# Kernel optimization log

Hardware: AMD Instinct MI355X
Metric: run time of the kernel (lower is better)

## Reference

```python
import jax, jax.numpy as jnp
import numpy as np

EMBED_DIM = 1024
NUM_HEADS = 16
HEAD_DIM = EMBED_DIM // NUM_HEADS
MLP_HIDDEN = 4096


def layer_norm(x, gamma, beta, eps=1e-5):
    mu = jnp.mean(x, axis=-1, keepdims=True)
    var = jnp.var(x, axis=-1, keepdims=True)
    return (x - mu) / jnp.sqrt(var + eps) * gamma + beta


def setup_inputs() -> dict:
    key = jax.random.key(0)
    ks = jax.random.split(key, 16)
    d, h = EMBED_DIM, MLP_HIDDEN
    s = 0.02
    inp = {
        "x": jax.random.normal(ks[0], (2, 2048, d), dtype=jnp.float32),
        "ln1_g": jnp.ones((d,), jnp.float32),
        "ln1_b": jnp.zeros((d,), jnp.float32),
        "ln2_g": jnp.ones((d,), jnp.float32),
        "ln2_b": jnp.zeros((d,), jnp.float32),
        "Wq": jax.random.normal(ks[1], (d, d), jnp.float32) * s,
        "bq": jnp.zeros((d,), jnp.float32),
        "Wk": jax.random.normal(ks[2], (d, d), jnp.float32) * s,
        "bk": jnp.zeros((d,), jnp.float32),
        "Wv": jax.random.normal(ks[3], (d, d), jnp.float32) * s,
        "bv": jnp.zeros((d,), jnp.float32),
        "Wo": jax.random.normal(ks[4], (d, d), jnp.float32) * s,
        "bo": jnp.zeros((d,), jnp.float32),
        "W1": jax.random.normal(ks[5], (d, h), jnp.float32) * s,
        "b1": jnp.zeros((h,), jnp.float32),
        "W2": jax.random.normal(ks[6], (h, d), jnp.float32) * s,
        "b2": jnp.zeros((d,), jnp.float32),
    }
    return inp


def reference(x, ln1_g, ln1_b, ln2_g, ln2_b, Wq, bq, Wk, bk, Wv, bv, Wo, bo, W1, b1, W2, b2):
    B, T, C = x.shape
    H, Dh = NUM_HEADS, HEAD_DIM
    # attention branch
    xn = layer_norm(x, ln1_g, ln1_b)
    q = (xn @ Wq + bq).reshape(B, T, H, Dh).transpose(0, 2, 1, 3)  # [B,H,T,Dh]
    k = (xn @ Wk + bk).reshape(B, T, H, Dh).transpose(0, 2, 1, 3)
    v = (xn @ Wv + bv).reshape(B, T, H, Dh).transpose(0, 2, 1, 3)
    scores = jnp.einsum('bhtd,bhsd->bhts', q, k) / jnp.sqrt(jnp.float32(Dh))
    attn = jax.nn.softmax(scores, axis=-1)
    out = jnp.einsum('bhts,bhsd->bhtd', attn, v)
    out = out.transpose(0, 2, 1, 3).reshape(B, T, C)
    x = x + out @ Wo + bo
    # MLP branch
    xn2 = layer_norm(x, ln2_g, ln2_b)
    x = x + jax.nn.relu(xn2 @ W1 + b1) @ W2 + b2
    return x
```

## Files before the change

kernel.cpp:

```cpp
#include <hip/hip_runtime.h>

typedef float f32x4 __attribute__((ext_vector_type(4)));
typedef __bf16 bf16x8 __attribute__((ext_vector_type(8)));

constexpr int TT   = 2048;
constexpr int CC   = 1024;
constexpr int HIDN = 4096;
constexpr int MM   = 4096;
constexpr int NQKV = 3072;

union U84 { uint32_t u[4]; bf16x8 v; };

__device__ inline uint32_t cvt_pk_bf16(float lo, float hi) {
  uint32_t r;
  asm("v_cvt_pk_bf16_f32 %0, %1, %2" : "=v"(r) : "v"(lo), "v"(hi));
  return r;
}
__device__ inline ushort f2bf(float f) { return (ushort)(cvt_pk_bf16(f, 0.f) & 0xffffu); }
__device__ inline float bfbits2f(uint32_t bits) {
  union { uint32_t u; float f; } c; c.u = bits; return c.f;
}
__device__ inline float exp2_fast(float x) {
  float r;
  asm("v_exp_f32 %0, %1" : "=v"(r) : "v"(x));
  return r;
}

#define AS1C(p) ((__attribute__((address_space(1))) void*)(p))
#define AS3(p)  ((__attribute__((address_space(3))) void*)(p))

__global__ __launch_bounds__(256) void prep_weights(const float* __restrict__ Wq,
                                                    const float* __restrict__ Wk,
                                                    const float* __restrict__ Wv,
                                                    const float* __restrict__ Wo,
                                                    const float* __restrict__ W1,
                                                    const float* __restrict__ W2,
                                                    const float* __restrict__ bq,
                                                    const float* __restrict__ bk,
                                                    const float* __restrict__ bv,
                                                    const float* __restrict__ x,
                                                    const float* __restrict__ g1,
                                                    const float* __restrict__ b1v,
                                                    ushort* __restrict__ WqkvT,
                                                    ushort* __restrict__ WoT,
                                                    ushort* __restrict__ W1T,
                                                    ushort* __restrict__ W2T,
                                                    float* __restrict__ Bqkv,
                                                    ushort* __restrict__ Xn) {
  const int id = blockIdx.x;
  const int t = threadIdx.x;
  if (id >= 12300) {
    const int row = id - 12300;
    float4 v = reinterpret_cast<const float4*>(x + (size_t)row * CC)[t];
    float s  = v.x + v.y + v.z + v.w;
    float ss = v.x * v.x + v.y * v.y + v.z * v.z + v.w * v.w;
#pragma unroll
    for (int off = 32; off; off >>= 1) {
      s  += __shfl_down(s, off);
      ss += __shfl_down(ss, off);
    }
    __shared__ float red[16];
    const int wid = t >> 6, lane = t & 63;
    if (lane == 0) { red[wid] = s; red[8 + wid] = ss; }
    __syncthreads();
    if (t == 0) {
      red[0] = red[0] + red[1] + red[2] + red[3];
      red[8] = red[8] + red[9] + red[10] + red[11];
    }
    __syncthreads();
    const float mu   = red[0] * (1.0f / CC);
    const float var  = red[8] * (1.0f / CC) - mu * mu;
    const float rstd = rsqrtf(var + 1e-5f);
    float4 gg = reinterpret_cast<const float4*>(g1)[t];
    float4 bb = reinterpret_cast<const float4*>(b1v)[t];
    uint2 st;
    st.x = cvt_pk_bf16((v.x - mu) * rstd * gg.x + bb.x, (v.y - mu) * rstd * gg.y + bb.y);
    st.y = cvt_pk_bf16((v.z - mu) * rstd * gg.z + bb.z, (v.w - mu) * rstd * gg.w + bb.w);
    *reinterpret_cast<uint2*>(Xn + (size_t)row * CC + t * 4) = st;
    return;
  }
  if (id >= 12288) {
    const int i = (id - 12288) * 256 + t;
    Bqkv[i] = (i < 1024) ? bq[i] : ((i < 2048) ? bk[i - 1024] : bv[i - 2048]);
    return;
  }
  const float* W; ushort* out; int Kd, Nd, bx, by, rowOff = 0;
  if (id < 4096) {
    const int which = id >> 10, sub = id & 1023;
    bx = sub & 31; by = sub >> 5; Kd = 1024; Nd = 1024;
    if (which == 0)      { W = Wq; out = WqkvT; rowOff = 0; }
    else if (which == 1) { W = Wk; out = WqkvT; rowOff = 1024; }
    else if (which == 2) { W = Wv; out = WqkvT; rowOff = 2048; }
    else                 { W = Wo; out = WoT; }
  } else if (id < 8192) {
    const int sub = id - 4096; bx = sub & 127; by = sub >> 7;
    W = W1; out = W1T; Kd = 1024; Nd = 4096;
  } else {
    const int sub = id - 8192; bx = sub & 31; by = sub >> 5;
    W = W2; out = W2T; Kd = 4096; Nd = 1024;
  }
  const int n0 = bx * 32, k0 = by * 32;
  __shared__ float Ts[32][33];
  {
    const int r = t >> 3, cb = (t & 7) * 4;
    float4 v = *reinterpret_cast<const float4*>(W + (size_t)(k0 + r) * Nd + n0 + cb);
    Ts[r][cb + 0] = v.x; Ts[r][cb + 1] = v.y; Ts[r][cb + 2] = v.z; Ts[r][cb + 3] = v.w;
  }
  __syncthreads();
  {
    const int nl = t >> 3, kb = (t & 7) * 4;
    uint2 st;
    st.x = cvt_pk_bf16(Ts[kb + 0][nl], Ts[kb + 1][nl]);
    st.y = cvt_pk_bf16(Ts[kb + 2][nl], Ts[kb + 3][nl]);
    *reinterpret_cast<uint2*>(out + (size_t)(rowOff + n0 + nl) * Kd + k0 + kb) = st;
  }
}

template <bool RELU, bool VOUT, bool PARTIAL>
__global__ __launch_bounds__(512, 2) void gemm_8w(const ushort* __restrict__ A,
                                                  const ushort* __restrict__ Bt,
                                                  const float* __restrict__ bias,
                                                  ushort* __restrict__ outp,
                                                  ushort* __restrict__ Vt,
                                                  ushort* __restrict__ P1,
                                                  ushort* __restrict__ P2,
                                                  ushort* __restrict__ P3,
                                                  int N, int K, int Kchunk) {
  __shared__ ushort lds[49152];
  const int t = threadIdx.x, lane = t & 63, w = t >> 6;
  const int g = lane >> 4, i16 = lane & 15;
  const int wr = w >> 2, wc = w & 3;
  const int nwg  = gridDim.x * gridDim.y;
  const int orig = blockIdx.y * gridDim.x + blockIdx.x;
  const int sw   = (orig & 7) * (nwg >> 3) + (orig >> 3);
  const int row0 = (sw / gridDim.x) * 256, col0 = (sw % gridDim.x) * 256;
  const int kstart = PARTIAL ? blockIdx.z * Kchunk : 0;
  const int NT = (PARTIAL ? Kchunk : K) >> 5;
  ushort* __restrict__ Out = outp;
  if (PARTIAL) Out = (blockIdx.z == 0) ? outp : (blockIdx.z == 1) ? P1
              : (blockIdx.z == 2) ? P2 : P3;

  const int c1 = t, c2 = t + 512;
  const int r1 = c1 >> 2, s1 = (c1 & 3) ^ ((r1 >> 1) & 3);
  const int r2 = c2 >> 2, s2 = (c2 & 3) ^ ((r2 >> 1) & 3);
  const ushort* aG1 = A + (size_t)(row0 + r1) * K + kstart + s1 * 8;
  const ushort* aG2 = A + (size_t)(row0 + r2) * K + kstart + s2 * 8;
  const ushort* bG1 = Bt + (size_t)(col0 + r1) * K + kstart + s1 * 8;
  const ushort* bG2 = Bt + (size_t)(col0 + r2) * K + kstart + s2 * 8;

  int aoff[8], boff[4];
#pragma unroll
  for (int mf = 0; mf < 8; ++mf) {
    const int R = wr * 128 + mf * 16 + i16;
    aoff[mf] = R * 64 + ((g ^ ((R >> 1) & 3)) << 4);
  }
#pragma unroll
  for (int nf = 0; nf < 4; ++nf) {
    const int Cn = wc * 64 + nf * 16 + i16;
    boff[nf] = Cn * 64 + ((g ^ ((Cn >> 1) & 3)) << 4);
  }

  f32x4 acc[8][4] = {};

  auto STAGE = [&](int bi, int kt) {
    char* aB = (char*)lds + bi * 32768;
    char* bB = aB + 16384;
    const int ko = kt * 32;
    __builtin_amdgcn_global_load_lds(AS1C(aG1 + ko), AS3(aB + w * 1024), 16, 0, 0);
    __builtin_amdgcn_global_load_lds(AS1C(aG2 + ko), AS3(aB + 8192 + w * 1024), 16, 0, 0);
    __builtin_amdgcn_global_load_lds(AS1C(bG1 + ko), AS3(bB + w * 1024), 16, 0, 0);
    __builtin_amdgcn_global_load_lds(AS1C(bG2 + ko), AS3(bB + 8192 + w * 1024), 16, 0, 0);
  };

  STAGE(0, 0);
  if (NT > 1) STAGE(1, 1);

  for (int kt = 0; kt < NT; ++kt) {
    const int cur = kt % 3;
    if (kt + 2 < NT) STAGE((kt + 2) % 3, kt + 2);
    if (kt + 2 < NT)      asm volatile("s_waitcnt vmcnt(8)" ::: "memory");
    else if (kt + 1 < NT) asm volatile("s_waitcnt vmcnt(4)" ::: "memory");
    else                  asm volatile("s_waitcnt vmcnt(0)" ::: "memory");
    asm volatile("s_barrier" ::: "memory");
    __builtin_amdgcn_sched_barrier(0);

    const char* aB = (const char*)lds + cur * 32768;
    const char* bB = aB + 16384;
    bf16x8 b4[4], a4[4];
#pragma unroll
    for (int nf = 0; nf < 4; ++nf) b4[nf] = *reinterpret_cast<const bf16x8*>(bB + boff[nf]);
#pragma unroll
    for (int mf = 0; mf < 4; ++mf) a4[mf] = *reinterpret_cast<const bf16x8*>(aB + aoff[mf]);
    __builtin_amdgcn_s_setprio(1);
#pragma unroll
    for (int mf = 0; mf < 4; ++mf)
#pragma unroll
      for (int nf = 0; nf < 4; ++nf)
        acc[mf][nf] = __builtin_amdgcn_mfma_f32_16x16x32_bf16(a4[mf], b4[nf], acc[mf][nf], 0, 0, 0);
    __builtin_amdgcn_s_setprio(0);
    asm volatile("s_barrier" ::: "memory");
    __builtin_amdgcn_sched_barrier(0);
#pragma unroll
    for (int mf = 0; mf < 4; ++mf) a4[mf] = *reinterpret_cast<const bf16x8*>(aB + aoff[mf + 4]);
    __builtin_amdgcn_s_setprio(1);
#pragma unroll
    for (int mf = 0; mf < 4; ++mf)
#pragma unroll
      for (int nf = 0; nf < 4; ++nf)
        acc[mf + 4][nf] = __builtin_amdgcn_mfma_f32_16x16x32_bf16(a4[mf], b4[nf], acc[mf + 4][nf], 0, 0, 0);
    __builtin_amdgcn_s_setprio(0);
    asm volatile("s_barrier" ::: "memory");
    __builtin_amdgcn_sched_barrier(0);
  }

  const int qcol0 = col0 + wc * 64;

  if (VOUT && qcol0 >= 2048) {
#pragma unroll
    for (int nf = 0; nf < 4; ++nf) {
      const int ncol = qcol0 + nf * 16 + i16;
      const float bb = bias[ncol];
      const int d = ncol - 2048;
      const int hh = d >> 6, dd = d & 63;
#pragma unroll
      for (int mf = 0; mf < 8; ++mf) {
        const int mrow = row0 + wr * 128 + mf * 16 + 4 * g;
        const int bb_ = mrow >> 11, tok = mrow & 2047;
        uint2 st;
        st.x = cvt_pk_bf16(acc[mf][nf][0] + bb, acc[mf][nf][1] + bb);
        st.y = cvt_pk_bf16(acc[mf][nf][2] + bb, acc[mf][nf][3] + bb);
        *reinterpret_cast<uint2*>(Vt + (size_t)((bb_ * 16 + hh) * 64 + dd) * TT + tok) = st;
      }
    }
    return;
  }

  float* Lf = (float*)((char*)lds + w * 4096);
  const int rr2 = lane >> 2, q = lane & 3;
#pragma unroll
  for (int mf = 0; mf < 8; ++mf) {
#pragma unroll
    for (int nf = 0; nf < 4; ++nf)
#pragma unroll
      for (int r = 0; r < 4; ++r) {
        const int row = 4 * g + r;
        Lf[row * 64 + ((16 * nf + i16) ^ ((row & 7) << 2))] = acc[mf][nf][r];
      }
    asm volatile("s_waitcnt lgkmcnt(0)" ::: "memory");
    uint32_t u[8];
#pragma unroll
    for (int j = 0; j < 4; ++j) {
      f32x4 v = *reinterpret_cast<const f32x4*>(Lf + rr2 * 64 + ((q * 16 + 4 * j) ^ ((rr2 & 7) << 2)));
      float e0 = v[0], e1 = v[1], e2 = v[2], e3 = v[3];
      if (!PARTIAL) {
        const float4 b4 = *reinterpret_cast<const float4*>(bias + qcol0 + q * 16 + 4 * j);
        e0 += b4.x; e1 += b4.y; e2 += b4.z; e3 += b4.w;
        if (RELU) {
          e0 = fmaxf(e0, 0.f); e1 = fmaxf(e1, 0.f);
          e2 = fmaxf(e2, 0.f); e3 = fmaxf(e3, 0.f);
        }
      }
      u[2 * j + 0] = cvt_pk_bf16(e0, e1);
      u[2 * j + 1] = cvt_pk_bf16(e2, e3);
    }
    const int mrow = row0 + wr * 128 + mf * 16 + rr2;
    ushort* orow = Out + (size_t)mrow * N + qcol0 + q * 16;
    uint4 s0; s0.x = u[0]; s0.y = u[1]; s0.z = u[2]; s0.w = u[3];
    uint4 s1; s1.x = u[4]; s1.y = u[5]; s1.z = u[6]; s1.w = u[7];
    *reinterpret_cast<uint4*>(orow) = s0;
    *reinterpret_cast<uint4*>(orow + 8) = s1;
    asm volatile("s_waitcnt lgkmcnt(0)" ::: "memory");
  }
}

__global__ __launch_bounds__(256) void gemm_splitk(const ushort* __restrict__ A,
                                                   const ushort* __restrict__ Bt,
                                                   ushort* __restrict__ P0,
                                                   ushort* __restrict__ P1,
                                                   ushort* __restrict__ P2,
                                                   ushort* __restrict__ P3,
                                                   int N, int K, int Kchunk) {
  __shared__ ushort Smem[8192];
  ushort* Asm = Smem;
  ushort* Bsm = Smem + 4096;
  const int t = threadIdx.x;
  const int lane = t & 63, w = t >> 6;
  const int g = lane >> 4, i16 = lane & 15;
  const int wrow = w >> 1, wcol = w & 1;
  const int nwg  = gridDim.x * gridDim.y;
  const int orig = blockIdx.y * gridDim.x + blockIdx.x;
  const int sw   = (orig & 7) * (nwg >> 3) + (orig >> 3);
  const int row0 = (sw / gridDim.x) * 128, col0 = (sw % gridDim.x) * 128;
  const int kstart = blockIdx.z * Kchunk;
  ushort* __restrict__ P = (blockIdx.z == 0) ? P0 : (blockIdx.z == 1) ? P1
                          : (blockIdx.z == 2) ? P2 : P3;

  f32x4 acc[4][4] = {};

  const int srow = t >> 2, sc = (t & 3) * 8;
  const ushort* aS1 = A + (size_t)(row0 + srow) * K + sc;
  const ushort* aS2 = A + (size_t)(row0 + 64 + srow) * K + sc;
  const ushort* bS1 = Bt + (size_t)(col0 + srow) * K + sc;
  const ushort* bS2 = Bt + (size_t)(col0 + 64 + srow) * K + sc;
  char* aL1 = (char*)Asm + w * 1024;
  char* aL2 = (char*)Asm + 4096 + w * 1024;
  char* bL1 = (char*)Bsm + w * 1024;
  char* bL2 = (char*)Bsm + 4096 + w * 1024;

  for (int k0 = kstart; k0 < kstart + Kchunk; k0 += 32) {
    __syncthreads();
    __builtin_amdgcn_global_load_lds(AS1C(aS1 + k0), AS3(aL1), 16, 0, 0);
    __builtin_amdgcn_global_load_lds(AS1C(aS2 + k0), AS3(aL2), 16, 0, 0);
    __builtin_amdgcn_global_load_lds(AS1C(bS1 + k0), AS3(bL1), 16, 0, 0);
    __builtin_amdgcn_global_load_lds(AS1C(bS2 + k0), AS3(bL2), 16, 0, 0);
    __syncthreads();

    bf16x8 a4[4], b4[4];
#pragma unroll
    for (int mf = 0; mf < 4; ++mf) {
      const int r = wrow * 64 + mf * 16 + i16;
      a4[mf] = *reinterpret_cast<const bf16x8*>((const char*)Asm + r * 64 + g * 16);
    }
#pragma unroll
    for (int nf = 0; nf < 4; ++nf) {
      const int c = wcol * 64 + nf * 16 + i16;
      b4[nf] = *reinterpret_cast<const bf16x8*>((const char*)Bsm + c * 64 + g * 16);
    }
#pragma unroll
    for (int mf = 0; mf < 4; ++mf)
#pragma unroll
      for (int nf = 0; nf < 4; ++nf)
        acc[mf][nf] = __builtin_amdgcn_mfma_f32_16x16x32_bf16(a4[mf], b4[nf], acc[mf][nf], 0, 0, 0);
  }

  __syncthreads();

  float* Lf = (float*)((char*)Smem + w * 4096);
  const int qcol0 = col0 + wcol * 64;
  const int rr = lane >> 2, q = lane & 3;
#pragma unroll
  for (int mf = 0; mf < 4; ++mf) {
#pragma unroll
    for (int nf = 0; nf < 4; ++nf)
#pragma unroll
      for (int r = 0; r < 4; ++r) {
        const int row = 4 * g + r;
        Lf[row * 64 + ((16 * nf + i16) ^ ((row & 7) << 2))] = acc[mf][nf][r];
      }
    asm volatile("s_waitcnt lgkmcnt(0)" ::: "memory");
    uint32_t u[8];
#pragma unroll
    for (int j = 0; j < 4; ++j) {
      f32x4 v = *reinterpret_cast<const f32x4*>(Lf + rr * 64 + ((q * 16 + 4 * j) ^ ((rr & 7) << 2)));
      u[2 * j + 0] = cvt_pk_bf16(v[0], v[1]);
      u[2 * j + 1] = cvt_pk_bf16(v[2], v[3]);
    }
    const int mrow = row0 + wrow * 64 + mf * 16 + rr;
    ushort* orow = P + (size_t)mrow * N + qcol0 + q * 16;
    uint4 s0; s0.x = u[0]; s0.y = u[1]; s0.z = u[2]; s0.w = u[3];
    uint4 s1; s1.x = u[4]; s1.y = u[5]; s1.z = u[6]; s1.w = u[7];
    *reinterpret_cast<uint4*>(orow) = s0;
    *reinterpret_cast<uint4*>(orow + 8) = s1;
    asm volatile("s_waitcnt lgkmcnt(0)" ::: "memory");
  }
}

__device__ inline float bfsum4(uint32_t a, uint32_t b, uint32_t c, uint32_t d, bool hi) {
  if (hi) return bfbits2f(a & 0xffff0000u) + bfbits2f(b & 0xffff0000u) +
                 bfbits2f(c & 0xffff0000u) + bfbits2f(d & 0xffff0000u);
  return bfbits2f(a << 16) + bfbits2f(b << 16) + bfbits2f(c << 16) + bfbits2f(d << 16);
}

__global__ __launch_bounds__(256) void reduce_wo_ln(const ushort* __restrict__ P0,
                                                    const ushort* __restrict__ P1,
                                                    const ushort* __restrict__ P2,
                                                    const ushort* __restrict__ P3,
                                                    const float* __restrict__ x,
                                                    const float* __restrict__ bo,
                                                    const float* __restrict__ g,
                                                    const float* __restrict__ b,
                                                    float* __restrict__ X1f,
                                                    ushort* __restrict__ Xn) {
  const int row = blockIdx.x, t = threadIdx.x;
  const size_t off = (size_t)row * CC + t * 4;
  float4 v  = *reinterpret_cast<const float4*>(x + off);
  const uint2 q0 = *reinterpret_cast<const uint2*>(P0 + off);
  const uint2 q1 = *reinterpret_cast<const uint2*>(P1 + off);
  const uint2 q2 = *reinterpret_cast<const uint2*>(P2 + off);
  const uint2 q3 = *reinterpret_cast<const uint2*>(P3 + off);
  float4 bb = reinterpret_cast<const float4*>(bo)[t];
  v.x += bfsum4(q0.x, q1.x, q2.x, q3.x, false) + bb.x;
  v.y += bfsum4(q0.x, q1.x, q2.x, q3.x, true)  + bb.y;
  v.z += bfsum4(q0.y, q1.y, q2.y, q3.y, false) + bb.z;
  v.w += bfsum4(q0.y, q1.y, q2.y, q3.y, true)  + bb.w;
  *reinterpret_cast<float4*>(X1f + off) = v;

  float s  = v.x + v.y + v.z + v.w;
  float ss = v.x * v.x + v.y * v.y + v.z * v.z + v.w * v.w;
#pragma unroll
  for (int o = 32; o; o >>= 1) {
    s  += __shfl_down(s, o);
    ss += __shfl_down(ss, o);
  }
  __shared__ float red[16];
  const int wid = t >> 6, lane = t & 63;
  if (lane == 0) { red[wid] = s; red[8 + wid] = ss; }
  __syncthreads();
  if (t == 0) {
    red[0] = red[0] + red[1] + red[2] + red[3];
    red[8] = red[8] + red[9] + red[10] + red[11];
  }
  __syncthreads();
  const float mu   = red[0] * (1.0f / CC);
  const float var  = red[8] * (1.0f / CC) - mu * mu;
  const float rstd = rsqrtf(var + 1e-5f);
  float4 gg = reinterpret_cast<const float4*>(g)[t];
  float4 lb = reinterpret_cast<const float4*>(b)[t];
  uint2 st;
  st.x = cvt_pk_bf16((v.x - mu) * rstd * gg.x + lb.x, (v.y - mu) * rstd * gg.y + lb.y);
  st.y = cvt_pk_bf16((v.z - mu) * rstd * gg.z + lb.z, (v.w - mu) * rstd * gg.w + lb.w);
  *reinterpret_cast<uint2*>(Xn + off) = st;
}

__global__ __launch_bounds__(256) void reduce_fc2(const ushort* __restrict__ P0,
                                                  const ushort* __restrict__ P1,
                                                  const ushort* __restrict__ P2,
                                                  const ushort* __restrict__ P3,
                                                  const float* __restrict__ X1,
                                                  const float* __restrict__ b2,
                                                  float* __restrict__ out) {
  const int row = blockIdx.x, t = threadIdx.x;
  const size_t off = (size_t)row * CC + t * 4;
  float4 v  = *reinterpret_cast<const float4*>(X1 + off);
  const uint2 q0 = *reinterpret_cast<const uint2*>(P0 + off);
  const uint2 q1 = *reinterpret_cast<const uint2*>(P1 + off);
  const uint2 q2 = *reinterpret_cast<const uint2*>(P2 + off);
  const uint2 q3 = *reinterpret_cast<const uint2*>(P3 + off);
  float4 bb = reinterpret_cast<const float4*>(b2)[t];
  v.x += bfsum4(q0.x, q1.x, q2.x, q3.x, false) + bb.x;
  v.y += bfsum4(q0.x, q1.x, q2.x, q3.x, true)  + bb.y;
  v.z += bfsum4(q0.y, q1.y, q2.y, q3.y, false) + bb.z;
  v.w += bfsum4(q0.y, q1.y, q2.y, q3.y, true)  + bb.w;
  *reinterpret_cast<float4*>(out + off) = v;
}

__global__ __launch_bounds__(512) void attn_partial(const ushort* __restrict__ qkv,
                                                    const ushort* __restrict__ Vt,
                                                    ushort* __restrict__ O0,
                                                    ushort* __restrict__ O1,
                                                    float2* __restrict__ ml) {
  __shared__ ushort Ks[64 * 64];
  __shared__ ushort Vs[64 * 64];
  __shared__ uint32_t Ps[8][16][36];
  const int t = threadIdx.x, lane = t & 63, w = t >> 6;
  const int g = lane >> 4, iq = lane & 15;
  const int flat = blockIdx.x;
  const int work = (flat & 7) * 128 + (flat >> 3);
  const int bh = work >> 5;
  const int rem = work & 31;
  const int z = rem >> 4;
  const int qt = rem & 15;
  const int b = bh >> 4, h = bh & 15;
  ushort* __restrict__ Obuf = z ? O1 : O0;

  bf16x8 qfrag[2];
  {
    const ushort* qrow = qkv + (size_t)(b * TT + qt * 128 + w * 16 + iq) * NQKV + h * 64;
    const float qs = 0.125f * 1.44269504f;
#pragma unroll
    for (int kk = 0; kk < 2; ++kk) {
      uint4 raw = *reinterpret_cast<const uint4*>(qrow + kk * 32 + g * 8);
      uint32_t rr[4] = {raw.x, raw.y, raw.z, raw.w};
      U84 tmp;
#pragma unroll
      for (int c = 0; c < 4; ++c) {
        float lo = bfbits2f(rr[c] << 16) * qs;
        float hi = bfbits2f(rr[c] & 0xffff0000u) * qs;
        tmp.u[c] = cvt_pk_bf16(lo, hi);
      }
      qfrag[kk] = tmp.v;
    }
  }

  const int sr1 = t >> 3, sc1 = t & 7;
  const int csw = (sc1 ^ (sr1 & 7)) * 8;
  const ushort* kbase = qkv + 1024 + h * 64;
  const ushort* vbase = Vt + (size_t)(bh * 64) * TT;
  char* kL = (char*)Ks + w * 1024;
  char* vL = (char*)Vs + w * 1024;

  uint32_t (*pw)[36] = Ps[w];
  const int wsw = (iq & 8) << 1;
  const int xsb = wsw << 2;
  const char* prow = (const char*)&pw[iq][0];

  float mrun = -3e38f, lrun = 0.f;
  f32x4 ot[4] = {};

  const int kt0 = z * 16;
  for (int kt = kt0; kt < kt0 + 16; ++kt) {
    __syncthreads();
    {
      const size_t tok = (size_t)(b * TT + kt * 64);
      __builtin_amdgcn_global_load_lds(AS1C(kbase + (tok + sr1) * NQKV + csw), AS3(kL), 16, 0, 0);
      __builtin_amdgcn_global_load_lds(AS1C(vbase + (size_t)sr1 * TT + kt * 64 + csw), AS3(vL), 16, 0, 0);
    }
    __syncthreads();

    f32x4 sfr[4] = {};
    __builtin_amdgcn_s_setprio(1);
#pragma unroll
    for (int kk = 0; kk < 2; ++kk)
#pragma unroll
      for (int jf = 0; jf < 4; ++jf) {
        const int row = iq + 16 * jf;
        const int off = row * 128 + ((kk * 64 + g * 16) ^ ((row & 7) << 4));
        bf16x8 a = *reinterpret_cast<const bf16x8*>((const char*)Ks + off);
        sfr[jf] = __builtin_amdgcn_mfma_f32_16x16x32_bf16(a, qfrag[kk], sfr[jf], 0, 0, 0);
      }
    __builtin_amdgcn_s_setprio(0);

    float tm0 = fmaxf(fmaxf(sfr[0][0], sfr[0][1]), fmaxf(sfr[0][2], sfr[0][3]));
    float tm1 = fmaxf(fmaxf(sfr[1][0], sfr[1][1]), fmaxf(sfr[1][2], sfr[1][3]));
    float tm2 = fmaxf(fmaxf(sfr[2][0], sfr[2][1]), fmaxf(sfr[2][2], sfr[2][3]));
    float tm3 = fmaxf(fmaxf(sfr[3][0], sfr[3][1]), fmaxf(sfr[3][2], sfr[3][3]));
    float tmax = fmaxf(fmaxf(tm0, tm1), fmaxf(tm2, tm3));
    tmax = fmaxf(tmax, __shfl_xor(tmax, 16, 64));
    tmax = fmaxf(tmax, __shfl_xor(tmax, 32, 64));

    if (!__all(tmax <= mrun + 8.f)) {
      const float mnew  = fmaxf(mrun, tmax);
      const float alpha = exp2_fast(mrun - mnew);
      lrun *= alpha;
#pragma unroll
      for (int df = 0; df < 4; ++df)
#pragma unroll
        for (int r = 0; r < 4; ++r) ot[df][r] *= alpha;
      mrun = mnew;
    }

#pragma unroll
    for (int f = 0; f < 4; ++f) {
      float p0 = exp2_fast(sfr[f][0] - mrun);
      float p1 = exp2_fast(sfr[f][1] - mrun);
      float p2 = exp2_fast(sfr[f][2] - mrun);
      float p3 = exp2_fast(sfr[f][3] - mrun);
      lrun += (p0 + p1) + (p2 + p3);
      pw[iq][(8 * f + 2 * g + 0) ^ wsw] = cvt_pk_bf16(p0, p1);
      pw[iq][(8 * f + 2 * g + 1) ^ wsw] = cvt_pk_bf16(p2, p3);
    }
    asm volatile("s_waitcnt lgkmcnt(0)" ::: "memory");

    __builtin_amdgcn_s_setprio(1);
#pragma unroll
    for (int kk = 0; kk < 2; ++kk) {
      bf16x8 pb = *reinterpret_cast<const bf16x8*>(prow + ((kk * 64 + g * 16) ^ xsb));
#pragma unroll
      for (int df = 0; df < 4; ++df) {
        const int row = iq + 16 * df;
        const int off = row * 128 + ((kk * 64 + g * 16) ^ ((row & 7) << 4));
        bf16x8 a = *reinterpret_cast<const bf16x8*>((const char*)Vs + off);
        ot[df] = __builtin_amdgcn_mfma_f32_16x16x32_bf16(a, pb, ot[df], 0, 0, 0);
      }
    }
    __builtin_amdgcn_s_setprio(0);
  }

  lrun += __shfl_xor(lrun, 16, 64);
  lrun += __shfl_xor(lrun, 32, 64);
  const int grow = b * TT + qt * 128 + w * 16 + iq;
  const float inv = 1.f / lrun;
  ushort* orow = Obuf + (size_t)grow * CC + h * 64;
#pragma unroll
  for (int df = 0; df < 4; ++df) {
    uint2 st;
    st.x = cvt_pk_bf16(ot[df][0] * inv, ot[df][1] * inv);
    st.y = cvt_pk_bf16(ot[df][2] * inv, ot[df][3] * inv);
    *reinterpret_cast<uint2*>(orow + df * 16 + g * 4) = st;
  }
  if (g == 0) ml[(size_t)z * (MM * 16) + grow * 16 + h] = make_float2(mrun, lrun);
}

__global__ __launch_bounds__(256) void attn_combine(const ushort* __restrict__ O0,
                                                    const ushort* __restrict__ O1,
                                                    const float2* __restrict__ ml,
                                                    ushort* __restrict__ attnb) {
  const int row = blockIdx.x, t = threadIdx.x;
  const int h = t >> 4;
  const float2 a = ml[(size_t)row * 16 + h];
  const float2 c = ml[(size_t)MM * 16 + (size_t)row * 16 + h];
  const float m  = fmaxf(a.x, c.x);
  const float w0 = exp2_fast(a.x - m) * a.y;
  const float w1 = exp2_fast(c.x - m) * c.y;
  const float inv = 1.f / (w0 + w1);
  const float s0 = w0 * inv, s1 = w1 * inv;
  const size_t off = (size_t)row * CC + t * 4;
  const uint2 r0 = *reinterpret_cast<const uint2*>(O0 + off);
  const uint2 r1 = *reinterpret_cast<const uint2*>(O1 + off);
  const float o0 = bfbits2f(r0.x << 16)         * s0 + bfbits2f(r1.x << 16)         * s1;
  const float o1 = bfbits2f(r0.x & 0xffff0000u) * s0 + bfbits2f(r1.x & 0xffff0000u) * s1;
  const float o2 = bfbits2f(r0.y << 16)         * s0 + bfbits2f(r1.y << 16)         * s1;
  const float o3 = bfbits2f(r0.y & 0xffff0000u) * s0 + bfbits2f(r1.y & 0xffff0000u) * s1;
  uint2 st;
  st.x = cvt_pk_bf16(o0, o1);
  st.y = cvt_pk_bf16(o2, o3);
  *reinterpret_cast<uint2*>(attnb + off) = st;
}

extern "C" void kernel_launch(void* const* d_in, const int* in_sizes, int n_in,
                              void* d_out, int out_size, void* d_ws, size_t ws_size,
                              hipStream_t stream) {
  const float* x     = (const float*)d_in[0];
  const float* ln1_g = (const float*)d_in[1];
  const float* ln1_b = (const float*)d_in[2];
  const float* ln2_g = (const float*)d_in[3];
  const float* ln2_b = (const float*)d_in[4];
  const float* Wq = (const float*)d_in[5];
  const float* bq = (const float*)d_in[6];
  const float* Wk = (const float*)d_in[7];
  const float* bk = (const float*)d_in[8];
  const float* Wv = (const float*)d_in[9];
  const float* bv = (const float*)d_in[10];
  const float* Wo = (const float*)d_in[11];
  const float* bo = (const float*)d_in[12];
  const float* W1 = (const float*)d_in[13];
  const float* b1 = (const float*)d_in[14];
  const float* W2 = (const float*)d_in[15];
  const float* b2 = (const float*)d_in[16];
  float* out = (float*)d_out;
  char* ws = (char*)d_ws;

  ushort* WqkvT = (ushort*)(ws + 0);
  ushort* WoT   = (ushort*)(ws + 6291456);
  ushort* W1T   = (ushort*)(ws + 8388608);
  ushort* W2T   = (ushort*)(ws + 16777216);
  float*  Bqkv  = (float*) (ws + 25165824);
  ushort* Xn    = (ushort*)(ws + 25178112);
  ushort* Attn  = (ushort*)(ws + 33566720);
  float*  X1f   = (float*) (ws + 41955328);
  ushort* Qkv   = (ushort*)(ws + 58732544);
  ushort* Vtb   = (ushort*)(ws + 83898368);
  ushort* Hid   = (ushort*)(ws + 58732544);
  ushort* OP0   = (ushort*)(ws + 41955328);
  ushort* OP1   = (ushort*)(ws + 50343936);
  float2* mlbuf = (float2*)(ws + 0);
  ushort* WoP0  = (ushort*)(ws + 58732544);
  ushort* WoP1  = (ushort*)(ws + 67121152);
  ushort* WoP2  = (ushort*)(ws + 75509760);
  ushort* WoP3  = (ushort*)(ws + 83898368);
  ushort* F2P0  = (ushort*)(ws + 0);
  ushort* F2P1  = (ushort*)(ws + 8388608);
  ushort* F2P2  = (ushort*)(ws + 25178112);
  ushort* F2P3  = (ushort*)(ws + 33566720);

  const dim3 blk(256);

  prep_weights<<<dim3(16396), blk, 0, stream>>>(Wq, Wk, Wv, Wo, W1, W2, bq, bk, bv,
                                                x, ln1_g, ln1_b,
                                                WqkvT, WoT, W1T, W2T, Bqkv, Xn);
  gemm_8w<false, true, false><<<dim3(12, 16), dim3(512), 0, stream>>>(
      Xn, WqkvT, Bqkv, Qkv, Vtb, nullptr, nullptr, nullptr, NQKV, 1024, 0);
  attn_partial<<<dim3(1024), dim3(512), 0, stream>>>(Qkv, Vtb, OP0, OP1, mlbuf);
  attn_combine<<<dim3(MM), blk, 0, stream>>>(OP0, OP1, mlbuf, Attn);
  gemm_splitk<<<dim3(8, 32, 4), blk, 0, stream>>>(Attn, WoT, WoP0, WoP1, WoP2, WoP3, 1024, 1024, 256);
  reduce_wo_ln<<<dim3(MM), blk, 0, stream>>>(WoP0, WoP1, WoP2, WoP3, x, bo, ln2_g, ln2_b, X1f, Xn);
  gemm_8w<true, false, false><<<dim3(16, 16), dim3(512), 0, stream>>>(
      Xn, W1T, b1, Hid, nullptr, nullptr, nullptr, nullptr, HIDN, 1024, 0);
  gemm_8w<false, false, true><<<dim3(4, 16, 4), dim3(512), 0, stream>>>(
      Hid, W2T, nullptr, F2P0, nullptr, F2P1, F2P2, F2P3, 1024, 4096, 1024);
  reduce_fc2<<<dim3(MM), blk, 0, stream>>>(F2P0, F2P1, F2P2, F2P3, X1f, b2, out);
}
```

Before: 257.8 us.

## Double-buffer K/V tiles and process two query sub-tiles per wave in attention

After: 255.9 us. About the same (-0.7%).

```diff
diff --git a/kernel.cpp b/kernel.cpp
--- a/kernel.cpp
+++ b/kernel.cpp
@@ -444,28 +444,29 @@
   *reinterpret_cast<float4*>(out + off) = v;
 }
 
-__global__ __launch_bounds__(512) void attn_partial(const ushort* __restrict__ qkv,
-                                                    const ushort* __restrict__ Vt,
-                                                    ushort* __restrict__ O0,
-                                                    ushort* __restrict__ O1,
-                                                    float2* __restrict__ ml) {
-  __shared__ ushort Ks[64 * 64];
-  __shared__ ushort Vs[64 * 64];
+__global__ __launch_bounds__(512, 4) void attn_partial(const ushort* __restrict__ qkv,
+                                                       const ushort* __restrict__ Vt,
+                                                       ushort* __restrict__ O0,
+                                                       ushort* __restrict__ O1,
+                                                       float2* __restrict__ ml) {
+  __shared__ ushort Ks[2][4096];
+  __shared__ ushort Vs[2][4096];
   __shared__ uint32_t Ps[8][16][36];
   const int t = threadIdx.x, lane = t & 63, w = t >> 6;
   const int g = lane >> 4, iq = lane & 15;
   const int flat = blockIdx.x;
-  const int work = (flat & 7) * 128 + (flat >> 3);
-  const int bh = work >> 5;
-  const int rem = work & 31;
-  const int z = rem >> 4;
-  const int qt = rem & 15;
+  const int work = (flat & 7) * 64 + (flat >> 3);
+  const int bh = work >> 4;
+  const int rem = work & 15;
+  const int z = rem >> 3;
+  const int qt = rem & 7;
   const int b = bh >> 4, h = bh & 15;
   ushort* __restrict__ Obuf = z ? O1 : O0;
 
-  bf16x8 qfrag[2];
-  {
-    const ushort* qrow = qkv + (size_t)(b * TT + qt * 128 + w * 16 + iq) * NQKV + h * 64;
+  bf16x8 qfrag[2][2];
+#pragma unroll
+  for (int qh = 0; qh < 2; ++qh) {
+    const ushort* qrow = qkv + (size_t)(b * TT + qt * 256 + w * 32 + qh * 16 + iq) * NQKV + h * 64;
     const float qs = 0.125f * 1.44269504f;
 #pragma unroll
     for (int kk = 0; kk < 2; ++kk) {
@@ -478,7 +479,7 @@
         float hi = bfbits2f(rr[c] & 0xffff0000u) * qs;
         tmp.u[c] = cvt_pk_bf16(lo, hi);
       }
-      qfrag[kk] = tmp.v;
+      qfrag[qh][kk] = tmp.v;
     }
   }
 
@@ -486,99 +487,121 @@
   const int csw = (sc1 ^ (sr1 & 7)) * 8;
   const ushort* kbase = qkv + 1024 + h * 64;
   const ushort* vbase = Vt + (size_t)(bh * 64) * TT;
-  char* kL = (char*)Ks + w * 1024;
-  char* vL = (char*)Vs + w * 1024;
+
+  auto STAGE = [&](int bi, int kt) {
+    const size_t tok = (size_t)(b * TT + kt * 64);
+    __builtin_amdgcn_global_load_lds(AS1C(kbase + (tok + sr1) * NQKV + csw),
+                                     AS3((char*)&Ks[bi][0] + w * 1024), 16, 0, 0);
+    __builtin_amdgcn_global_load_lds(AS1C(vbase + (size_t)sr1 * TT + kt * 64 + csw),
+                                     AS3((char*)&Vs[bi][0] + w * 1024), 16, 0, 0);
+  };
 
   uint32_t (*pw)[36] = Ps[w];
   const int wsw = (iq & 8) << 1;
   const int xsb = wsw << 2;
   const char* prow = (const char*)&pw[iq][0];
 
-  float mrun = -3e38f, lrun = 0.f;
-  f32x4 ot[4] = {};
-
-  const int kt0 = z * 16;
-  for (int kt = kt0; kt < kt0 + 16; ++kt) {
-    __syncthreads();
-    {
-      const size_t tok = (size_t)(b * TT + kt * 64);
-      __builtin_amdgcn_global_load_lds(AS1C(kbase + (tok + sr1) * NQKV + csw), AS3(kL), 16, 0, 0);
-      __builtin_amdgcn_global_load_lds(AS1C(vbase + (size_t)sr1 * TT + kt * 64 + csw), AS3(vL), 16, 0, 0);
-    }
-    __syncthreads();
-
-    f32x4 sfr[4] = {};
-    __builtin_amdgcn_s_setprio(1);
-#pragma unroll
-    for (int kk = 0; kk < 2; ++kk)
-#pragma unroll
-      for (int jf = 0; jf < 4; ++jf) {
-        const int row = iq + 16 * jf;
-        const int off = row * 128 + ((kk * 64 + g * 16) ^ ((row & 7) << 4));
-        bf16x8 a = *reinterpret_cast<const bf16x8*>((const char*)Ks + off);
-        sfr[jf] = __builtin_amdgcn_mfma_f32_16x16x32_bf16(a, qfrag[kk], sfr[jf], 0, 0, 0);
-      }
-    __builtin_amdgcn_s_setprio(0);
-
-    float tm0 = fmaxf(fmaxf(sfr[0][0], sfr[0][1]), fmaxf(sfr[0][2], sfr[0][3]));
-    float tm1 = fmaxf(fmaxf(sfr[1][0], sfr[1][1]), fmaxf(sfr[1][2], sfr[1][3]));
-    float tm2 = fmaxf(fmaxf(sfr[2][0], sfr[2][1]), fmaxf(sfr[2][2], sfr[2][3]));
-    float tm3 = fmaxf(fmaxf(sfr[3][0], sfr[3][1]), fmaxf(sfr[3][2], sfr[3][3]));
-    float tmax = fmaxf(fmaxf(tm0, tm1), fmaxf(tm2, tm3));
-    tmax = fmaxf(tmax, __shfl_xor(tmax, 16, 64));
-    tmax = fmaxf(tmax, __shfl_xor(tmax, 32, 64));
-
-    if (!__all(tmax <= mrun + 8.f)) {
-      const float mnew  = fmaxf(mrun, tmax);
-      const float alpha = exp2_fast(mrun - mnew);
-      lrun *= alpha;
-#pragma unroll
-      for (int df = 0; df < 4; ++df)
-#pragma unroll
-        for (int r = 0; r < 4; ++r) ot[df][r] *= alpha;
-      mrun = mnew;
-    }
-
-#pragma unroll
-    for (int f = 0; f < 4; ++f) {
-      float p0 = exp2_fast(sfr[f][0] - mrun);
-      float p1 = exp2_fast(sfr[f][1] - mrun);
-      float p2 = exp2_fast(sfr[f][2] - mrun);
-      float p3 = exp2_fast(sfr[f][3] - mrun);
-      lrun += (p0 + p1) + (p2 + p3);
-      pw[iq][(8 * f + 2 * g + 0) ^ wsw] = cvt_pk_bf16(p0, p1);
-      pw[iq][(8 * f + 2 * g + 1) ^ wsw] = cvt_pk_bf16(p2, p3);
-    }
-    asm volatile("s_waitcnt lgkmcnt(0)" ::: "memory");
-
-    __builtin_amdgcn_s_setprio(1);
-#pragma unroll
-    for (int kk = 0; kk < 2; ++kk) {
-      bf16x8 pb = *reinterpret_cast<const bf16x8*>(prow + ((kk * 64 + g * 16) ^ xsb));
-#pragma unroll
-      for (int df = 0; df < 4; ++df) {
-        const int row = iq + 16 * df;
-        const int off = row * 128 + ((kk * 64 + g * 16) ^ ((row & 7) << 4));
-        bf16x8 a = *reinterpret_cast<const bf16x8*>((const char*)Vs + off);
-        ot[df] = __builtin_amdgcn_mfma_f32_16x16x32_bf16(a, pb, ot[df], 0, 0, 0);
-      }
-    }
-    __builtin_amdgcn_s_setprio(0);
-  }
-
-  lrun += __shfl_xor(lrun, 16, 64);
-  lrun += __shfl_xor(lrun, 32, 64);
-  const int grow = b * TT + qt * 128 + w * 16 + iq;
-  const float inv = 1.f / lrun;
-  ushort* orow = Obuf + (size_t)grow * CC + h * 64;
-#pragma unroll
-  for (int df = 0; df < 4; ++df) {
-    uint2 st;
-    st.x = cvt_pk_bf16(ot[df][0] * inv, ot[df][1] * inv);
-    st.y = cvt_pk_bf16(ot[df][2] * inv, ot[df][3] * inv);
-    *reinterpret_cast<uint2*>(orow + df * 16 + g * 4) = st;
-  }
-  if (g == 0) ml[(size_t)z * (MM * 16) + grow * 16 + h] = make_float2(mrun, lrun);
+  float mrun[2] = {-3e38f, -3e38f}, lrun[2] = {0.f, 0.f};
+  f32x4 ot[2][4] = {};
+
+  const int kt0 = z * 16, ktE = kt0 + 16;
+  STAGE(0, kt0);
+
+  for (int kt = kt0; kt < ktE; ++kt) {
+    const int cur = kt & 1;
+    if (kt + 1 < ktE) {
+      STAGE(cur ^ 1, kt + 1);
+      asm volatile("s_waitcnt vmcnt(2)" ::: "memory");
+    } else {
+      asm volatile("s_waitcnt vmcnt(0)" ::: "memory");
+    }
+    asm volatile("s_barrier" ::: "memory");
+    __builtin_amdgcn_sched_barrier(0);
+    const char* Kc = (const char*)&Ks[cur][0];
+    const char* Vc = (const char*)&Vs[cur][0];
+
+#pragma unroll
+    for (int qh = 0; qh < 2; ++qh) {
+      f32x4 sfr[4] = {};
+      __builtin_amdgcn_s_setprio(1);
+#pragma unroll
+      for (int kk = 0; kk < 2; ++kk)
+#pragma unroll
+        for (int jf = 0; jf < 4; ++jf) {
+          const int row = iq + 16 * jf;
+          const int off = row * 128 + ((kk * 64 + g * 16) ^ ((row & 7) << 4));
+          bf16x8 a = *reinterpret_cast<const bf16x8*>(Kc + off);
+          sfr[jf] = __builtin_amdgcn_mfma_f32_16x16x32_bf16(a, qfrag[qh][kk], sfr[jf], 0, 0, 0);
+        }
+      __builtin_amdgcn_s_setprio(0);
+
+      float tm0 = fmaxf(fmaxf(sfr[0][0], sfr[0][1]), fmaxf(sfr[0][2], sfr[0][3]));
+      float tm1 = fmaxf(fmaxf(sfr[1][0], sfr[1][1]), fmaxf(sfr[1][2], sfr[1][3]));
+      float tm2 = fmaxf(fmaxf(sfr[2][0], sfr[2][1]), fmaxf(sfr[2][2], sfr[2][3]));
+      float tm3 = fmaxf(fmaxf(sfr[3][0], sfr[3][1]), fmaxf(sfr[3][2], sfr[3][3]));
+      float tmax = fmaxf(fmaxf(tm0, tm1), fmaxf(tm2, tm3));
+      tmax = fmaxf(tmax, __shfl_xor(tmax, 16, 64));
+      tmax = fmaxf(tmax, __shfl_xor(tmax, 32, 64));
+
+      if (!__all(tmax <= mrun[qh] + 8.f)) {
+        const float mnew  = fmaxf(mrun[qh], tmax);
+        const float alpha = exp2_fast(mrun[qh] - mnew);
+        lrun[qh] *= alpha;
+#pragma unroll
+        for (int df = 0; df < 4; ++df)
+#pragma unroll
+          for (int r = 0; r < 4; ++r) ot[qh][df][r] *= alpha;
+        mrun[qh] = mnew;
+      }
+
+#pragma unroll
+      for (int f = 0; f < 4; ++f) {
+        float p0 = exp2_fast(sfr[f][0] - mrun[qh]);
+        float p1 = exp2_fast(sfr[f][1] - mrun[qh]);
+        float p2 = exp2_fast(sfr[f][2] - mrun[qh]);
+        float p3 = exp2_fast(sfr[f][3] - mrun[qh]);
+        lrun[qh] += (p0 + p1) + (p2 + p3);
+        pw[iq][(8 * f + 2 * g + 0) ^ wsw] = cvt_pk_bf16(p0, p1);
+        pw[iq][(8 * f + 2 * g + 1) ^ wsw] = cvt_pk_bf16(p2, p3);
+      }
+      asm volatile("s_waitcnt lgkmcnt(0)" ::: "memory");
+
+      __builtin_amdgcn_s_setprio(1);
+#pragma unroll
+      for (int kk = 0; kk < 2; ++kk) {
+        bf16x8 pb = *reinterpret_cast<const bf16x8*>(prow + ((kk * 64 + g * 16) ^ xsb));
+#pragma unroll
+        for (int df = 0; df < 4; ++df) {
+          const int row = iq + 16 * df;
+          const int off = row * 128 + ((kk * 64 + g * 16) ^ ((row & 7) << 4));
+          bf16x8 a = *reinterpret_cast<const bf16x8*>(Vc + off);
+          ot[qh][df] = __builtin_amdgcn_mfma_f32_16x16x32_bf16(a, pb, ot[qh][df], 0, 0, 0);
+        }
+      }
+      __builtin_amdgcn_s_setprio(0);
+    }
+
+    asm volatile("s_barrier" ::: "memory");
+    __builtin_amdgcn_sched_barrier(0);
+  }
+
+#pragma unroll
+  for (int qh = 0; qh < 2; ++qh) {
+    float l = lrun[qh];
+    l += __shfl_xor(l, 16, 64);
+    l += __shfl_xor(l, 32, 64);
+    const int grow = b * TT + qt * 256 + w * 32 + qh * 16 + iq;
+    const float inv = 1.f / l;
+    ushort* orow = Obuf + (size_t)grow * CC + h * 64;
+#pragma unroll
+    for (int df = 0; df < 4; ++df) {
+      uint2 st;
+      st.x = cvt_pk_bf16(ot[qh][df][0] * inv, ot[qh][df][1] * inv);
+      st.y = cvt_pk_bf16(ot[qh][df][2] * inv, ot[qh][df][3] * inv);
+      *reinterpret_cast<uint2*>(orow + df * 16 + g * 4) = st;
+    }
+    if (g == 0) ml[(size_t)z * (MM * 16) + (size_t)grow * 16 + h] = make_float2(mrun[qh], l);
+  }
 }
 
 __global__ __launch_bounds__(256) void attn_combine(const ushort* __restrict__ O0,
@@ -660,7 +683,7 @@
                                                 WqkvT, WoT, W1T, W2T, Bqkv, Xn);
   gemm_8w<false, true, false><<<dim3(12, 16), dim3(512), 0, stream>>>(
       Xn, WqkvT, Bqkv, Qkv, Vtb, nullptr, nullptr, nullptr, NQKV, 1024, 0);
-  attn_partial<<<dim3(1024), dim3(512), 0, stream>>>(Qkv, Vtb, OP0, OP1, mlbuf);
+  attn_partial<<<dim3(512), dim3(512), 0, stream>>>(Qkv, Vtb, OP0, OP1, mlbuf);
   attn_combine<<<dim3(MM), blk, 0, stream>>>(OP0, OP1, mlbuf, Attn);
   gemm_splitk<<<dim3(8, 32, 4), blk, 0, stream>>>(Attn, WoT, WoP0, WoP1, WoP2, WoP3, 1024, 1024, 256);
   reduce_wo_ln<<<dim3(MM), blk, 0, stream>>>(WoP0, WoP1, WoP2, WoP3, x, bo, ln2_g, ln2_b, X1f, Xn);
```

## Replace split-KV attention plus combine with single-pass double-buffered attention kernel

Applied to the files above, without the earlier changes.

After: 252.6 us. -2.0%, faster.

```diff
diff --git a/kernel.cpp b/kernel.cpp
--- a/kernel.cpp
+++ b/kernel.cpp
@@ -444,24 +444,19 @@
   *reinterpret_cast<float4*>(out + off) = v;
 }
 
-__global__ __launch_bounds__(512) void attn_partial(const ushort* __restrict__ qkv,
+__global__ __launch_bounds__(512, 4) void attn_full(const ushort* __restrict__ qkv,
                                                     const ushort* __restrict__ Vt,
-                                                    ushort* __restrict__ O0,
-                                                    ushort* __restrict__ O1,
-                                                    float2* __restrict__ ml) {
-  __shared__ ushort Ks[64 * 64];
-  __shared__ ushort Vs[64 * 64];
+                                                    ushort* __restrict__ attnb) {
+  __shared__ ushort Ks[2][4096];
+  __shared__ ushort Vs[2][4096];
   __shared__ uint32_t Ps[8][16][36];
   const int t = threadIdx.x, lane = t & 63, w = t >> 6;
   const int g = lane >> 4, iq = lane & 15;
   const int flat = blockIdx.x;
-  const int work = (flat & 7) * 128 + (flat >> 3);
-  const int bh = work >> 5;
-  const int rem = work & 31;
-  const int z = rem >> 4;
-  const int qt = rem & 15;
+  const int work = (flat & 7) * 64 + (flat >> 3);
+  const int bh = work >> 4;
+  const int qt = work & 15;
   const int b = bh >> 4, h = bh & 15;
-  ushort* __restrict__ Obuf = z ? O1 : O0;
 
   bf16x8 qfrag[2];
   {
@@ -486,8 +481,14 @@
   const int csw = (sc1 ^ (sr1 & 7)) * 8;
   const ushort* kbase = qkv + 1024 + h * 64;
   const ushort* vbase = Vt + (size_t)(bh * 64) * TT;
-  char* kL = (char*)Ks + w * 1024;
-  char* vL = (char*)Vs + w * 1024;
+
+  auto STAGE = [&](int bi, int kt) {
+    const size_t tok = (size_t)(b * TT + kt * 64);
+    __builtin_amdgcn_global_load_lds(AS1C(kbase + (tok + sr1) * NQKV + csw),
+                                     AS3((char*)&Ks[bi][0] + w * 1024), 16, 0, 0);
+    __builtin_amdgcn_global_load_lds(AS1C(vbase + (size_t)sr1 * TT + kt * 64 + csw),
+                                     AS3((char*)&Vs[bi][0] + w * 1024), 16, 0, 0);
+  };
 
   uint32_t (*pw)[36] = Ps[w];
   const int wsw = (iq & 8) << 1;
@@ -497,15 +498,21 @@
   float mrun = -3e38f, lrun = 0.f;
   f32x4 ot[4] = {};
 
-  const int kt0 = z * 16;
-  for (int kt = kt0; kt < kt0 + 16; ++kt) {
-    __syncthreads();
-    {
-      const size_t tok = (size_t)(b * TT + kt * 64);
-      __builtin_amdgcn_global_load_lds(AS1C(kbase + (tok + sr1) * NQKV + csw), AS3(kL), 16, 0, 0);
-      __builtin_amdgcn_global_load_lds(AS1C(vbase + (size_t)sr1 * TT + kt * 64 + csw), AS3(vL), 16, 0, 0);
-    }
-    __syncthreads();
+  constexpr int NKT = TT / 64;
+  STAGE(0, 0);
+
+  for (int kt = 0; kt < NKT; ++kt) {
+    const int cur = kt & 1;
+    if (kt + 1 < NKT) {
+      STAGE(cur ^ 1, kt + 1);
+      asm volatile("s_waitcnt vmcnt(2)" ::: "memory");
+    } else {
+      asm volatile("s_waitcnt vmcnt(0)" ::: "memory");
+    }
+    asm volatile("s_barrier" ::: "memory");
+    __builtin_amdgcn_sched_barrier(0);
+    const char* Kc = (const char*)&Ks[cur][0];
+    const char* Vc = (const char*)&Vs[cur][0];
 
     f32x4 sfr[4] = {};
     __builtin_amdgcn_s_setprio(1);
@@ -515,7 +522,7 @@
       for (int jf = 0; jf < 4; ++jf) {
         const int row = iq + 16 * jf;
         const int off = row * 128 + ((kk * 64 + g * 16) ^ ((row & 7) << 4));
-        bf16x8 a = *reinterpret_cast<const bf16x8*>((const char*)Ks + off);
+        bf16x8 a = *reinterpret_cast<const bf16x8*>(Kc + off);
         sfr[jf] = __builtin_amdgcn_mfma_f32_16x16x32_bf16(a, qfrag[kk], sfr[jf], 0, 0, 0);
       }
     __builtin_amdgcn_s_setprio(0);
@@ -559,18 +566,21 @@
       for (int df = 0; df < 4; ++df) {
         const int row = iq + 16 * df;
         const int off = row * 128 + ((kk * 64 + g * 16) ^ ((row & 7) << 4));
-        bf16x8 a = *reinterpret_cast<const bf16x8*>((const char*)Vs + off);
+        bf16x8 a = *reinterpret_cast<const bf16x8*>(Vc + off);
         ot[df] = __builtin_amdgcn_mfma_f32_16x16x32_bf16(a, pb, ot[df], 0, 0, 0);
       }
     }
     __builtin_amdgcn_s_setprio(0);
+
+    asm volatile("s_barrier" ::: "memory");
+    __builtin_amdgcn_sched_barrier(0);
   }
 
   lrun += __shfl_xor(lrun, 16, 64);
   lrun += __shfl_xor(lrun, 32, 64);
   const int grow = b * TT + qt * 128 + w * 16 + iq;
   const float inv = 1.f / lrun;
-  ushort* orow = Obuf + (size_t)grow * CC + h * 64;
+  ushort* orow = attnb + (size_t)grow * CC + h * 64;
 #pragma unroll
   for (int df = 0; df < 4; ++df) {
     uint2 st;
@@ -578,33 +588,6 @@
     st.y = cvt_pk_bf16(ot[df][2] * inv, ot[df][3] * inv);
     *reinterpret_cast<uint2*>(orow + df * 16 + g * 4) = st;
   }
-  if (g == 0) ml[(size_t)z * (MM * 16) + grow * 16 + h] = make_float2(mrun, lrun);
-}
-
-__global__ __launch_bounds__(256) void attn_combine(const ushort* __restrict__ O0,
-                                                    const ushort* __restrict__ O1,
-                                                    const float2* __restrict__ ml,
-                                                    ushort* __restrict__ attnb) {
-  const int row = blockIdx.x, t = threadIdx.x;
-  const int h = t >> 4;
-  const float2 a = ml[(size_t)row * 16 + h];
-  const float2 c = ml[(size_t)MM * 16 + (size_t)row * 16 + h];
-  const float m  = fmaxf(a.x, c.x);
-  const float w0 = exp2_fast(a.x - m) * a.y;
-  const float w1 = exp2_fast(c.x - m) * c.y;
-  const float inv = 1.f / (w0 + w1);
-  const float s0 = w0 * inv, s1 = w1 * inv;
-  const size_t off = (size_t)row * CC + t * 4;
-  const uint2 r0 = *reinterpret_cast<const uint2*>(O0 + off);
-  const uint2 r1 = *reinterpret_cast<const uint2*>(O1 + off);
-  const float o0 = bfbits2f(r0.x << 16)         * s0 + bfbits2f(r1.x << 16)         * s1;
-  const float o1 = bfbits2f(r0.x & 0xffff0000u) * s0 + bfbits2f(r1.x & 0xffff0000u) * s1;
-  const float o2 = bfbits2f(r0.y << 16)         * s0 + bfbits2f(r1.y << 16)         * s1;
-  const float o3 = bfbits2f(r0.y & 0xffff0000u) * s0 + bfbits2f(r1.y & 0xffff0000u) * s1;
-  uint2 st;
-  st.x = cvt_pk_bf16(o0, o1);
-  st.y = cvt_pk_bf16(o2, o3);
-  *reinterpret_cast<uint2*>(attnb + off) = st;
 }
 
 extern "C" void kernel_launch(void* const* d_in, const int* in_sizes, int n_in,
@@ -641,9 +624,6 @@
   ushort* Qkv   = (ushort*)(ws + 58732544);
   ushort* Vtb   = (ushort*)(ws + 83898368);
   ushort* Hid   = (ushort*)(ws + 58732544);
-  ushort* OP0   = (ushort*)(ws + 41955328);
-  ushort* OP1   = (ushort*)(ws + 50343936);
-  float2* mlbuf = (float2*)(ws + 0);
   ushort* WoP0  = (ushort*)(ws + 58732544);
   ushort* WoP1  = (ushort*)(ws + 67121152);
   ushort* WoP2  = (ushort*)(ws + 75509760);
@@ -660,8 +640,7 @@
                                                 WqkvT, WoT, W1T, W2T, Bqkv, Xn);
   gemm_8w<false, true, false><<<dim3(12, 16), dim3(512), 0, stream>>>(
       Xn, WqkvT, Bqkv, Qkv, Vtb, nullptr, nullptr, nullptr, NQKV, 1024, 0);
-  attn_partial<<<dim3(1024), dim3(512), 0, stream>>>(Qkv, Vtb, OP0, OP1, mlbuf);
-  attn_combine<<<dim3(MM), blk, 0, stream>>>(OP0, OP1, mlbuf, Attn);
+  attn_full<<<dim3(512), dim3(512), 0, stream>>>(Qkv, Vtb, Attn);
   gemm_splitk<<<dim3(8, 32, 4), blk, 0, stream>>>(Attn, WoT, WoP0, WoP1, WoP2, WoP3, 1024, 1024, 256);
   reduce_wo_ln<<<dim3(MM), blk, 0, stream>>>(WoP0, WoP1, WoP2, WoP3, x, bo, ln2_g, ln2_b, X1f, Xn);
   gemm_8w<true, false, false><<<dim3(16, 16), dim3(512), 0, stream>>>(
```
